# Performance work log

Measured on AMD Instinct MI355X. Metric: run time of the kernel, lower is better.

The kernel has to match this reference:

```python
import jax, jax.numpy as jnp
import numpy as np

B, H, W, C = 4, 256, 256, 128
HEADS, WS, SHIFT = 4, 8, 4
EPS = 1e-5


def _rel_pos_index(ws):
    coords = np.stack(np.meshgrid(np.arange(ws), np.arange(ws), indexing='ij'))
    cf = coords.reshape(2, -1)
    rel = (cf[:, :, None] - cf[:, None, :]).transpose(1, 2, 0)
    rel[:, :, 0] += ws - 1
    rel[:, :, 1] += ws - 1
    rel[:, :, 0] *= 2 * ws - 1
    return rel.sum(-1).reshape(-1)

REL_IDX = jnp.array(_rel_pos_index(WS))


def _shift_mask(h, w, ws, shift):
    img = np.zeros((1, h, w, 1))
    cnt = 0
    sl = (slice(0, -ws), slice(-ws, -shift), slice(-shift, None))
    for hs in sl:
        for wsl in sl:
            img[:, hs, wsl, :] = cnt
            cnt += 1
    m = img.reshape(1, h // ws, ws, w // ws, ws, 1).transpose(0, 1, 3, 2, 4, 5).reshape(-1, ws * ws)
    am = m[:, None, :] - m[:, :, None]
    return jnp.array(np.where(am != 0, -100.0, 0.0).astype(np.float32))

ATTN_MASK = _shift_mask(H, W, WS, SHIFT)  # (nW, ws*ws, ws*ws)


def _ln(x, scale, bias):
    mu = x.mean(-1, keepdims=True)
    var = x.var(-1, keepdims=True)
    return (x - mu) / jnp.sqrt(var + EPS) * scale + bias


def setup_inputs() -> dict:
    key = jax.random.key(0)
    ks = jax.random.split(key, 8)
    s = 0.02
    return dict(
        hidden_states=jax.random.normal(ks[0], (B, H * W, C), jnp.float32),
        ln1_scale=jnp.ones((C,), jnp.float32), ln1_bias=jnp.zeros((C,), jnp.float32),
        q_w=jax.random.normal(ks[1], (C, C), jnp.float32) * s, q_b=jnp.zeros((C,), jnp.float32),
        k_w=jax.random.normal(ks[2], (C, C), jnp.float32) * s, k_b=jnp.zeros((C,), jnp.float32),
        v_w=jax.random.normal(ks[3], (C, C), jnp.float32) * s, v_b=jnp.zeros((C,), jnp.float32),
        proj_w=jax.random.normal(ks[4], (C, C), jnp.float32) * s, proj_b=jnp.zeros((C,), jnp.float32),
        rpb_table=jax.random.normal(ks[5], ((2 * WS - 1) ** 2, HEADS), jnp.float32) * s,
        ln2_scale=jnp.ones((C,), jnp.float32), ln2_bias=jnp.zeros((C,), jnp.float32),
        fc1_w=jax.random.normal(ks[6], (C, 4 * C), jnp.float32) * s, fc1_b=jnp.zeros((4 * C,), jnp.float32),
        fc2_w=jax.random.normal(ks[7], (4 * C, C), jnp.float32) * s, fc2_b=jnp.zeros((C,), jnp.float32),
    )


def reference(hidden_states, ln1_scale, ln1_bias, q_w, q_b, k_w, k_b, v_w, v_b,
              proj_w, proj_b, rpb_table, ln2_scale, ln2_bias, fc1_w, fc1_b, fc2_w, fc2_b):
    hd = C // HEADS
    T = WS * WS
    nW = (H // WS) * (W // WS)
    shortcut = hidden_states
    x = _ln(hidden_states, ln1_scale, ln1_bias).reshape(B, H, W, C)
    # cyclic shift
    x = jnp.roll(x, (-SHIFT, -SHIFT), axis=(1, 2))
    # window partition -> (B*nW, T, C)
    x = x.reshape(B, H // WS, WS, W // WS, WS, C).transpose(0, 1, 3, 2, 4, 5).reshape(-1, T, C)
    q = (x @ q_w + q_b).reshape(-1, T, HEADS, hd) / jnp.sqrt(jnp.float32(hd))
    k = (x @ k_w + k_b).reshape(-1, T, HEADS, hd)
    v = (x @ v_w + v_b).reshape(-1, T, HEADS, hd)
    attn = jnp.einsum('bqhd,bkhd->bhqk', q, k)
    bias = rpb_table[REL_IDX].reshape(T, T, HEADS).transpose(2, 0, 1)  # (h, q, k)
    attn = attn + bias[None]
    # shift mask per window
    attn = attn.reshape(B, nW, HEADS, T, T) + ATTN_MASK[None, :, None]
    attn = jax.nn.softmax(attn.reshape(-1, HEADS, T, T), axis=-1)
    out = jnp.einsum('bhqk,bkhd->bqhd', attn, v).reshape(-1, T, C)
    out = out @ proj_w + proj_b
    # window reverse + un-shift
    out = out.reshape(B, H // WS, W // WS, WS, WS, C).transpose(0, 1, 3, 2, 4, 5).reshape(B, H, W, C)
    out = jnp.roll(out, (SHIFT, SHIFT), axis=(1, 2)).reshape(B, H * W, C)
    x = shortcut + out
    y = _ln(x, ln2_scale, ln2_bias)
    y = jax.nn.gelu(y @ fc1_w + fc1_b, approximate=False) @ fc2_w + fc2_b
    return x + y
```

## Files before the change

kernel.cpp:

```cpp
#include <hip/hip_runtime.h>
#include <hip/hip_bf16.h>
#include <math.h>

#define B_ 4
#define H_ 256
#define W_ 256
#define C_ 128
#define HEADS_ 4
#define HD_ 32
#define WS_ 8
#define SHIFT_ 4
#define T_ 64
#define NW_ 1024
#define M_ (B_*NW_*T_)

typedef float floatx4 __attribute__((ext_vector_type(4)));
typedef short bf16x8 __attribute__((ext_vector_type(8)));
typedef unsigned short ushort8v __attribute__((ext_vector_type(8)));

#define MFMA16(a,b,c) __builtin_amdgcn_mfma_f32_16x16x32_bf16(a,b,c,0,0,0)

__device__ __forceinline__ unsigned short f2b(float f){
    union { float f; unsigned int i; } c; c.f = f;
    unsigned int r = c.i + 0x7FFFu + ((c.i >> 16) & 1u);
    return (unsigned short)(r >> 16);
}
__device__ __forceinline__ int region_id(int x){ return (x < 248) ? 0 : ((x < 252) ? 1 : 2); }

__device__ __forceinline__ bf16x8 ldfrag(const unsigned short* p){
    return *(const bf16x8*)p;
}
__device__ __forceinline__ bf16x8 ldfrag_strided(const unsigned short* p, int stride){
    ushort8v u;
    #pragma unroll
    for (int j = 0; j < 8; j++) u[j] = p[j*stride];
    return __builtin_bit_cast(bf16x8, u);
}
__device__ __forceinline__ floatx4 fzero(){ floatx4 v = {0.f,0.f,0.f,0.f}; return v; }

__device__ __forceinline__ float gelu_fast(float x){
    float z = x * 0.70710678118654752f;
    float az = fabsf(z);
    float t = __builtin_amdgcn_rcpf(fmaf(0.3275911f, az, 1.0f));
    float poly = t*(0.254829592f + t*(-0.284496736f + t*(1.421413741f +
                 t*(-1.453152027f + t*1.061405429f))));
    float e = __expf(-z*z);
    float er = 1.0f - poly*e;
    er = (z < 0.f) ? -er : er;
    return 0.5f * x * (1.0f + er);
}

#define WSO_QT   0
#define WSO_KT   16384
#define WSO_VT   32768
#define WSO_PT   49152
#define WSO_W1T  65536
#define WSO_W2T  131072
#define WSO_BIAS 196608
#define WS_BYTES_NEEDED (196608u*2u + 16384u*4u)

__global__ __launch_bounds__(256) void prep_weights_kernel(
        const float* __restrict__ qw, const float* __restrict__ kw,
        const float* __restrict__ vw, const float* __restrict__ pw,
        const float* __restrict__ fc1, const float* __restrict__ fc2,
        const float* __restrict__ rpb, unsigned short* __restrict__ ws)
{
    int tid = blockIdx.x * 256 + threadIdx.x;
    int nt = gridDim.x * 256;
    for (int i = tid; i < 16384; i += nt) {
        int n = i >> 7, k = i & 127;
        ws[WSO_QT + i] = f2b(qw[k*128 + n]);
        ws[WSO_KT + i] = f2b(kw[k*128 + n]);
        ws[WSO_VT + i] = f2b(vw[k*128 + n]);
        ws[WSO_PT + i] = f2b(pw[k*128 + n]);
    }
    for (int i = tid; i < 65536; i += nt) {
        int n = i >> 7, k = i & 127;
        ws[WSO_W1T + i] = f2b(fc1[(size_t)k*512 + n]);
    }
    for (int i = tid; i < 65536; i += nt) {
        int n = i >> 9, k = i & 511;
        ws[WSO_W2T + i] = f2b(fc2[(size_t)k*128 + n]);
    }
    float* bt = (float*)(ws + WSO_BIAS);
    for (int i = tid; i < 16384; i += nt) {
        int h = i >> 12, q = (i >> 6) & 63, k = i & 63;
        int th = q >> 3, tw = q & 7, jh = k >> 3, jw = k & 7;
        bt[i] = rpb[((th - jh + 7)*15 + (tw - jw + 7))*HEADS_ + h];
    }
}

__device__ __forceinline__ void gemm64x128_g(
        const unsigned short (*Xs)[136], const unsigned short* __restrict__ Wt,
        int wv, int quad, int l15, floatx4 acc[4][2])
{
    #pragma unroll
    for (int c = 0; c < 4; c++) {
        bf16x8 bf0 = ldfrag(Wt + (size_t)(32*wv + l15)*128      + c*32 + quad*8);
        bf16x8 bf1 = ldfrag(Wt + (size_t)(32*wv + 16 + l15)*128 + c*32 + quad*8);
        #pragma unroll
        for (int m = 0; m < 4; m++) {
            bf16x8 af = ldfrag(&Xs[16*m + l15][c*32 + quad*8]);
            acc[m][0] = MFMA16(af, bf0, acc[m][0]);
            acc[m][1] = MFMA16(af, bf1, acc[m][1]);
        }
    }
}

__global__ __launch_bounds__(256, 3) void swin_fused_kernel(
        const float* __restrict__ hidden,
        const float* __restrict__ ln1_s, const float* __restrict__ ln1_b,
        const float* __restrict__ q_b, const float* __restrict__ k_b,
        const float* __restrict__ v_b, const float* __restrict__ p_b,
        const float* __restrict__ ln2_s, const float* __restrict__ ln2_b,
        const float* __restrict__ b1, const float* __restrict__ b2,
        const unsigned short* __restrict__ wsu,
        float* __restrict__ outp)
{
    __shared__ __align__(16) unsigned short SH[2][T_][136];
    __shared__ __align__(16) unsigned short VsT[C_][72];
    unsigned short (*Xs)[136] = SH[0];
    unsigned short (*Ks)[136] = SH[1];

    int tid = threadIdx.x;
    int wv = tid >> 6, lane = tid & 63;
    int quad = lane >> 4, l15 = lane & 15;
    int gw = blockIdx.x;
    int wi = gw & (NW_-1), b = gw >> 10;
    int hb = wi >> 5, wb = wi & 31;

    {
        int rloc = lane >> 2;
        int t = wv*16 + rloc;
        int th = t >> 3, tw = t & 7;
        int h = (hb*8 + th + SHIFT_) & 255;
        int w = (wb*8 + tw + SHIFT_) & 255;
        int c0 = (lane & 3) * 32;
        const float* xp = hidden + ((size_t)((b<<16) + (h<<8) + w)) * C_ + c0;
        float4 xv[8];
        float s = 0.f, ss = 0.f;
        #pragma unroll
        for (int i = 0; i < 8; i++) {
            xv[i] = *((const float4*)xp + i);
            s  += xv[i].x + xv[i].y + xv[i].z + xv[i].w;
            ss += xv[i].x*xv[i].x + xv[i].y*xv[i].y + xv[i].z*xv[i].z + xv[i].w*xv[i].w;
        }
        s  += __shfl_xor(s, 1, 64);  s  += __shfl_xor(s, 2, 64);
        ss += __shfl_xor(ss, 1, 64); ss += __shfl_xor(ss, 2, 64);
        float mean = s * (1.0f/C_);
        float var  = ss * (1.0f/C_) - mean*mean;
        float rstd = __builtin_amdgcn_rsqf(var + 1e-5f);
        #pragma unroll
        for (int i = 0; i < 8; i++) {
            float4 sc = *((const float4*)(ln1_s + c0) + i);
            float4 bi = *((const float4*)(ln1_b + c0) + i);
            ushort4 o;
            o.x = f2b((xv[i].x - mean)*rstd*sc.x + bi.x);
            o.y = f2b((xv[i].y - mean)*rstd*sc.y + bi.y);
            o.z = f2b((xv[i].z - mean)*rstd*sc.z + bi.z);
            o.w = f2b((xv[i].w - mean)*rstd*sc.w + bi.w);
            *(ushort4*)&Xs[t][c0 + 4*i] = o;
        }
    }
    __syncthreads();

    floatx4 qacc[4][2];
    {
        floatx4 kacc[4][2], vacc[4][2];
        #pragma unroll
        for (int m = 0; m < 4; m++) {
            qacc[m][0] = fzero(); qacc[m][1] = fzero();
            kacc[m][0] = fzero(); kacc[m][1] = fzero();
            vacc[m][0] = fzero(); vacc[m][1] = fzero();
        }
        const unsigned short* Qt = wsu + WSO_QT;
        const unsigned short* Kt = wsu + WSO_KT;
        const unsigned short* Vt = wsu + WSO_VT;
        #pragma unroll
        for (int c = 0; c < 4; c++) {
            size_t off0 = (size_t)(32*wv + l15)*128      + c*32 + quad*8;
            size_t off1 = (size_t)(32*wv + 16 + l15)*128 + c*32 + quad*8;
            bf16x8 qf0 = ldfrag(Qt + off0), qf1 = ldfrag(Qt + off1);
            bf16x8 kf0 = ldfrag(Kt + off0), kf1 = ldfrag(Kt + off1);
            bf16x8 vf0 = ldfrag(Vt + off0), vf1 = ldfrag(Vt + off1);
            #pragma unroll
            for (int m = 0; m < 4; m++) {
                bf16x8 af = ldfrag(&Xs[16*m + l15][c*32 + quad*8]);
                qacc[m][0] = MFMA16(af, qf0, qacc[m][0]);
                qacc[m][1] = MFMA16(af, qf1, qacc[m][1]);
                kacc[m][0] = MFMA16(af, kf0, kacc[m][0]);
                kacc[m][1] = MFMA16(af, kf1, kacc[m][1]);
                vacc[m][0] = MFMA16(af, vf0, vacc[m][0]);
                vacc[m][1] = MFMA16(af, vf1, vacc[m][1]);
            }
        }
        float kb0 = k_b[32*wv + l15], kb1 = k_b[32*wv + 16 + l15];
        float vb0 = v_b[32*wv + l15], vb1 = v_b[32*wv + 16 + l15];
        #pragma unroll
        for (int m = 0; m < 4; m++)
            #pragma unroll
            for (int r = 0; r < 4; r++) {
                int q = 16*m + 4*quad + r;
                Ks[q][32*wv + l15]      = f2b(kacc[m][0][r] + kb0);
                Ks[q][32*wv + 16 + l15] = f2b(kacc[m][1][r] + kb1);
                VsT[32*wv + l15][q]      = f2b(vacc[m][0][r] + vb0);
                VsT[32*wv + 16 + l15][q] = f2b(vacc[m][1][r] + vb1);
            }
    }
    __syncthreads();
    {
        const float sc = 0.17677669529663687f;
        float qb0 = q_b[32*wv + l15], qb1 = q_b[32*wv + 16 + l15];
        #pragma unroll
        for (int m = 0; m < 4; m++)
            #pragma unroll
            for (int r = 0; r < 4; r++) {
                int q = 16*m + 4*quad + r;
                Xs[q][32*wv + l15]      = f2b((qacc[m][0][r] + qb0) * sc);
                Xs[q][32*wv + 16 + l15] = f2b((qacc[m][1][r] + qb1) * sc);
            }
    }

    floatx4 sacc[4][4];
    #pragma unroll
    for (int m = 0; m < 4; m++)
        #pragma unroll
        for (int n = 0; n < 4; n++) sacc[m][n] = fzero();
    {
        bf16x8 qf[4], kf[4];
        #pragma unroll
        for (int m = 0; m < 4; m++) qf[m] = ldfrag(&Xs[16*m + l15][32*wv + quad*8]);
        #pragma unroll
        for (int n = 0; n < 4; n++) kf[n] = ldfrag(&Ks[16*n + l15][32*wv + quad*8]);
        #pragma unroll
        for (int m = 0; m < 4; m++)
            #pragma unroll
            for (int n = 0; n < 4; n++) sacc[m][n] = MFMA16(kf[n], qf[m], sacc[m][n]);
    }

    {
        const float* bt = (const float*)(wsu + WSO_BIAS) + (wv << 12);
        int cidk[4][4];
        #pragma unroll
        for (int n = 0; n < 4; n++)
            #pragma unroll
            for (int r = 0; r < 4; r++) {
                int kt = 16*n + 4*quad + r;
                cidk[n][r] = region_id(hb*8 + (kt >> 3))*3 + region_id(wb*8 + (kt & 7));
            }
        #pragma unroll
        for (int m = 0; m < 4; m++) {
            int q = 16*m + l15;
            int cidq = region_id(hb*8 + (q >> 3))*3 + region_id(wb*8 + (q & 7));
            float v[4][4];
            float mx = -3.0e38f;
            #pragma unroll
            for (int n = 0; n < 4; n++) {
                float4 bv = *(const float4*)(bt + q*64 + 16*n + 4*quad);
                #pragma unroll
                for (int r = 0; r < 4; r++) {
                    float d = sacc[m][n][r] + bv[r];
                    if (cidq != cidk[n][r]) d -= 100.f;
                    v[n][r] = d;
                    mx = fmaxf(mx, d);
                }
            }
            mx = fmaxf(mx, __shfl_xor(mx, 16, 64));
            mx = fmaxf(mx, __shfl_xor(mx, 32, 64));
            float sum = 0.f;
            #pragma unroll
            for (int n = 0; n < 4; n++)
                #pragma unroll
                for (int r = 0; r < 4; r++) { v[n][r] = __expf(v[n][r] - mx); sum += v[n][r]; }
            sum += __shfl_xor(sum, 16, 64);
            sum += __shfl_xor(sum, 32, 64);
            float inv = __builtin_amdgcn_rcpf(sum);
            #pragma unroll
            for (int n = 0; n < 4; n++)
                #pragma unroll
                for (int r = 0; r < 4; r++) sacc[m][n][r] = v[n][r] * inv;
        }
    }
    __syncthreads();

    unsigned short* Ph = (wv < 2) ? (&Ks[0][0] + wv*2560) : (&Xs[0][0] + (wv-2)*2560);
    floatx4 oacc[4][2];
    #pragma unroll
    for (int m = 0; m < 4; m++) { oacc[m][0] = fzero(); oacc[m][1] = fzero(); }
    #pragma unroll
    for (int kb = 0; kb < 2; kb++) {
        #pragma unroll
        for (int m = 0; m < 4; m++)
            #pragma unroll
            for (int n2 = 0; n2 < 2; n2++)
                #pragma unroll
                for (int r = 0; r < 4; r++)
                    Ph[(16*m + l15)*40 + n2*16 + 4*quad + r] = f2b(sacc[m][2*kb + n2][r]);
        bf16x8 bf0 = ldfrag(&VsT[32*wv + l15][kb*32 + quad*8]);
        bf16x8 bf1 = ldfrag(&VsT[32*wv + 16 + l15][kb*32 + quad*8]);
        #pragma unroll
        for (int m = 0; m < 4; m++) {
            bf16x8 af = ldfrag(&Ph[(16*m + l15)*40 + quad*8]);
            oacc[m][0] = MFMA16(af, bf0, oacc[m][0]);
            oacc[m][1] = MFMA16(af, bf1, oacc[m][1]);
        }
    }
    __syncthreads();
    #pragma unroll
    for (int m = 0; m < 4; m++)
        #pragma unroll
        for (int r = 0; r < 4; r++) {
            int q = 16*m + 4*quad + r;
            Xs[q][32*wv + l15]      = f2b(oacc[m][0][r]);
            Xs[q][32*wv + 16 + l15] = f2b(oacc[m][1][r]);
        }
    __syncthreads();

    floatx4 pacc[4][2];
    #pragma unroll
    for (int m = 0; m < 4; m++) { pacc[m][0] = fzero(); pacc[m][1] = fzero(); }
    gemm64x128_g(Xs, wsu + WSO_PT, wv, quad, l15, pacc);
    {
        float pb0 = p_b[32*wv + l15], pb1 = p_b[32*wv + 16 + l15];
        #pragma unroll
        for (int m = 0; m < 4; m++)
            #pragma unroll
            for (int r = 0; r < 4; r++) {
                int t = 16*m + 4*quad + r;
                int th = t >> 3, tw = t & 7;
                int h = (hb*8 + th + SHIFT_) & 255;
                int w = (wb*8 + tw + SHIFT_) & 255;
                size_t src = ((size_t)((b<<16) + (h<<8) + w)) * C_;
                pacc[m][0][r] += pb0 + hidden[src + 32*wv + l15];
                pacc[m][1][r] += pb1 + hidden[src + 32*wv + 16 + l15];
            }
    }
    __syncthreads();

    float* Fb = (float*)&SH[0][0][0];
    #pragma unroll
    for (int m = 0; m < 4; m++)
        #pragma unroll
        for (int r = 0; r < 4; r++) {
            int q = 16*m + 4*quad + r;
            Fb[q*132 + 32*wv + l15]      = pacc[m][0][r];
            Fb[q*132 + 32*wv + 16 + l15] = pacc[m][1][r];
        }
    __syncthreads();

    unsigned short (*As)[136] = (unsigned short(*)[136])&VsT[0][0];
    {
        int rloc = lane >> 2;
        int t = wv*16 + rloc;
        int c0 = (lane & 3) * 32;
        const float* xp = Fb + t*132 + c0;
        float4 xv[8];
        float s = 0.f, ss = 0.f;
        #pragma unroll
        for (int i = 0; i < 8; i++) {
            xv[i] = *((const float4*)xp + i);
            s  += xv[i].x + xv[i].y + xv[i].z + xv[i].w;
            ss += xv[i].x*xv[i].x + xv[i].y*xv[i].y + xv[i].z*xv[i].z + xv[i].w*xv[i].w;
        }
        s  += __shfl_xor(s, 1, 64);  s  += __shfl_xor(s, 2, 64);
        ss += __shfl_xor(ss, 1, 64); ss += __shfl_xor(ss, 2, 64);
        float mean = s * (1.0f/C_);
        float var  = ss * (1.0f/C_) - mean*mean;
        float rstd = __builtin_amdgcn_rsqf(var + 1e-5f);
        #pragma unroll
        for (int i = 0; i < 8; i++) {
            float4 sc = *((const float4*)(ln2_s + c0) + i);
            float4 bi = *((const float4*)(ln2_b + c0) + i);
            ushort4 o;
            o.x = f2b((xv[i].x - mean)*rstd*sc.x + bi.x);
            o.y = f2b((xv[i].y - mean)*rstd*sc.y + bi.y);
            o.z = f2b((xv[i].z - mean)*rstd*sc.z + bi.z);
            o.w = f2b((xv[i].w - mean)*rstd*sc.w + bi.w);
            *(ushort4*)&As[t][c0 + 4*i] = o;
        }
    }
    __syncthreads();

    unsigned short (*G)[72] = (unsigned short(*)[72])&SH[0][0][0];
    const unsigned short* W1t = wsu + WSO_W1T;
    const unsigned short* W2t = wsu + WSO_W2T;
    floatx4 acc2[4][2];
    #pragma unroll
    for (int m = 0; m < 4; m++) { acc2[m][0] = fzero(); acc2[m][1] = fzero(); }

    for (int ch = 0; ch < 8; ch++) {
        floatx4 a1[4];
        #pragma unroll
        for (int m = 0; m < 4; m++) a1[m] = fzero();
        #pragma unroll
        for (int kc = 0; kc < 4; kc++) {
            bf16x8 bf = ldfrag(W1t + (size_t)(ch*64 + 16*wv + l15)*128 + kc*32 + quad*8);
            #pragma unroll
            for (int m = 0; m < 4; m++) {
                bf16x8 af = ldfrag(&As[16*m + l15][kc*32 + quad*8]);
                a1[m] = MFMA16(af, bf, a1[m]);
            }
        }
        __syncthreads();
        {
            int c_rel = 16*wv + l15;
            float bb = b1[ch*64 + c_rel];
            #pragma unroll
            for (int m = 0; m < 4; m++)
                #pragma unroll
                for (int r = 0; r < 4; r++) {
                    float hh = a1[m][r] + bb;
                    G[16*m + 4*quad + r][c_rel] = f2b(gelu_fast(hh));
                }
        }
        __syncthreads();
        #pragma unroll
        for (int ki = 0; ki < 2; ki++) {
            bf16x8 bf0 = ldfrag(W2t + (size_t)(32*wv + l15)*512      + ch*64 + ki*32 + quad*8);
            bf16x8 bf1 = ldfrag(W2t + (size_t)(32*wv + 16 + l15)*512 + ch*64 + ki*32 + quad*8);
            #pragma unroll
            for (int m = 0; m < 4; m++) {
                bf16x8 af = ldfrag(&G[16*m + l15][ki*32 + quad*8]);
                acc2[m][0] = MFMA16(af, bf0, acc2[m][0]);
                acc2[m][1] = MFMA16(af, bf1, acc2[m][1]);
            }
        }
    }
    __syncthreads();

    {
        float bb0 = b2[32*wv + l15], bb1 = b2[32*wv + 16 + l15];
        #pragma unroll
        for (int m = 0; m < 4; m++)
            #pragma unroll
            for (int r = 0; r < 4; r++) {
                int q = 16*m + 4*quad + r;
                Fb[q*132 + 32*wv + l15]      = pacc[m][0][r] + acc2[m][0][r] + bb0;
                Fb[q*132 + 32*wv + 16 + l15] = pacc[m][1][r] + acc2[m][1][r] + bb1;
            }
        __syncthreads();
        int t = tid >> 2;
        int cs = (tid & 3) * 32;
        int th = t >> 3, tw = t & 7;
        int h = (hb*8 + th + SHIFT_) & 255;
        int w = (wb*8 + tw + SHIFT_) & 255;
        size_t dst = ((size_t)((b<<16) + (h<<8) + w)) * C_ + cs;
        float4* op = (float4*)(outp + dst);
        const float4* fp = (const float4*)(Fb + t*132 + cs);
        #pragma unroll
        for (int i = 0; i < 8; i++) op[i] = fp[i];
    }
}


__device__ __forceinline__ void gemm64x128(
        const unsigned short (*Xs)[136], unsigned short (*Wc)[132],
        const float* __restrict__ Wg, int tid, int wv, int quad, int l15,
        floatx4 acc[4][2])
{
    for (int c = 0; c < 4; c++) {
        __syncthreads();
        #pragma unroll
        for (int it = 0; it < 4; it++) {
            int idx = tid + it*256;
            int kk = idx >> 5;
            int n4 = (idx & 31) * 4;
            float4 v = *(const float4*)(Wg + (size_t)(c*32 + kk)*C_ + n4);
            ushort4 o; o.x=f2b(v.x); o.y=f2b(v.y); o.z=f2b(v.z); o.w=f2b(v.w);
            *(ushort4*)&Wc[kk][n4] = o;
        }
        __syncthreads();
        bf16x8 bf0 = ldfrag_strided(&Wc[quad*8][32*wv + l15],      132);
        bf16x8 bf1 = ldfrag_strided(&Wc[quad*8][32*wv + 16 + l15], 132);
        #pragma unroll
        for (int m = 0; m < 4; m++) {
            bf16x8 af = ldfrag(&Xs[16*m + l15][c*32 + quad*8]);
            acc[m][0] = MFMA16(af, bf0, acc[m][0]);
            acc[m][1] = MFMA16(af, bf1, acc[m][1]);
        }
    }
}

__global__ __launch_bounds__(256) void swin_attn_kernel(
        const float* __restrict__ hidden,
        const float* __restrict__ ln1_s, const float* __restrict__ ln1_b,
        const float* __restrict__ q_w, const float* __restrict__ q_b,
        const float* __restrict__ k_w, const float* __restrict__ k_b,
        const float* __restrict__ v_w, const float* __restrict__ v_b,
        const float* __restrict__ p_w, const float* __restrict__ p_b,
        const float* __restrict__ rpb,
        float* __restrict__ xres)
{
    __shared__ unsigned short Xs[T_][136];
    __shared__ unsigned short Ks[T_][136];
    __shared__ unsigned short Vs[T_][134];
    __shared__ __align__(16) unsigned char U[10240];

    unsigned short (*Wc)[132] = (unsigned short(*)[132])U;
    float* rpbf = (float*)U;

    int tid = threadIdx.x;
    int wv = tid >> 6, lane = tid & 63;
    int quad = lane >> 4, l15 = lane & 15;
    int gw = blockIdx.x;
    int wi = gw & (NW_-1), b = gw >> 10;
    int hb = wi >> 5, wb = wi & 31;

    for (int it = 0; it < 16; it++) {
        int t = wv*16 + it;
        int th = t >> 3, tw = t & 7;
        int h = (hb*8 + th + SHIFT_) & 255;
        int w = (wb*8 + tw + SHIFT_) & 255;
        size_t src = ((size_t)((b<<16) + (h<<8) + w)) * C_;
        float2 u = *(const float2*)(hidden + src + 2*lane);
        float x0 = u.x, x1 = u.y;
        float s = x0 + x1, ss = x0*x0 + x1*x1;
        #pragma unroll
        for (int m = 32; m > 0; m >>= 1) {
            s  += __shfl_xor(s,  m, 64);
            ss += __shfl_xor(ss, m, 64);
        }
        float mean = s * (1.0f/C_);
        float var  = ss * (1.0f/C_) - mean*mean;
        float rstd = rsqrtf(var + 1e-5f);
        int c0 = 2*lane;
        ushort2 o;
        o.x = f2b((x0 - mean) * rstd * ln1_s[c0]   + ln1_b[c0]);
        o.y = f2b((x1 - mean) * rstd * ln1_s[c0+1] + ln1_b[c0+1]);
        *(ushort2*)&Xs[t][c0] = o;
    }

    {
        floatx4 acc[4][2];
        #pragma unroll
        for (int m = 0; m < 4; m++) { acc[m][0] = fzero(); acc[m][1] = fzero(); }
        gemm64x128(Xs, Wc, k_w, tid, wv, quad, l15, acc);
        float kb0 = k_b[32*wv + l15], kb1 = k_b[32*wv + 16 + l15];
        #pragma unroll
        for (int m = 0; m < 4; m++)
            #pragma unroll
            for (int r = 0; r < 4; r++) {
                int q = 16*m + 4*quad + r;
                Ks[q][32*wv + l15]      = f2b(acc[m][0][r] + kb0);
                Ks[q][32*wv + 16 + l15] = f2b(acc[m][1][r] + kb1);
            }
    }
    {
        floatx4 acc[4][2];
        #pragma unroll
        for (int m = 0; m < 4; m++) { acc[m][0] = fzero(); acc[m][1] = fzero(); }
        gemm64x128(Xs, Wc, v_w, tid, wv, quad, l15, acc);
        float vb0 = v_b[32*wv + l15], vb1 = v_b[32*wv + 16 + l15];
        #pragma unroll
        for (int m = 0; m < 4; m++)
            #pragma unroll
            for (int r = 0; r < 4; r++) {
                int q = 16*m + 4*quad + r;
                Vs[q][32*wv + l15]      = f2b(acc[m][0][r] + vb0);
                Vs[q][32*wv + 16 + l15] = f2b(acc[m][1][r] + vb1);
            }
    }
    floatx4 qacc[4][2];
    #pragma unroll
    for (int m = 0; m < 4; m++) { qacc[m][0] = fzero(); qacc[m][1] = fzero(); }
    gemm64x128(Xs, Wc, q_w, tid, wv, quad, l15, qacc);
    __syncthreads();
    for (int i = tid; i < 225*HEADS_; i += 256) rpbf[i] = rpb[i];
    {
        const float sc = 0.17677669529663687f;
        float qb0 = q_b[32*wv + l15], qb1 = q_b[32*wv + 16 + l15];
        #pragma unroll
        for (int m = 0; m < 4; m++)
            #pragma unroll
            for (int r = 0; r < 4; r++) {
                int q = 16*m + 4*quad + r;
                Xs[q][32*wv + l15]      = f2b((qacc[m][0][r] + qb0) * sc);
                Xs[q][32*wv + 16 + l15] = f2b((qacc[m][1][r] + qb1) * sc);
            }
    }
    __syncthreads();

    floatx4 sacc[4][4];
    #pragma unroll
    for (int m = 0; m < 4; m++)
        #pragma unroll
        for (int n = 0; n < 4; n++) sacc[m][n] = fzero();
    {
        bf16x8 qf[4], kf[4];
        #pragma unroll
        for (int m = 0; m < 4; m++) qf[m] = ldfrag(&Xs[16*m + l15][32*wv + quad*8]);
        #pragma unroll
        for (int n = 0; n < 4; n++) kf[n] = ldfrag(&Ks[16*n + l15][32*wv + quad*8]);
        #pragma unroll
        for (int m = 0; m < 4; m++)
            #pragma unroll
            for (int n = 0; n < 4; n++) sacc[m][n] = MFMA16(qf[m], kf[n], sacc[m][n]);
    }
    {
        int jh_[4], jw_[4], cidj_[4];
        #pragma unroll
        for (int n = 0; n < 4; n++) {
            int kt = 16*n + l15;
            jh_[n] = kt >> 3; jw_[n] = kt & 7;
            cidj_[n] = region_id(hb*8 + jh_[n])*3 + region_id(wb*8 + jw_[n]);
        }
        #pragma unroll
        for (int m = 0; m < 4; m++)
            #pragma unroll
            for (int r = 0; r < 4; r++) {
                int q = 16*m + 4*quad + r;
                int th = q >> 3, twq = q & 7;
                int cidi = region_id(hb*8 + th)*3 + region_id(wb*8 + twq);
                float v[4];
                #pragma unroll
                for (int n = 0; n < 4; n++) {
                    float d = sacc[m][n][r];
                    d += rpbf[((th - jh_[n] + 7)*15 + (twq - jw_[n] + 7))*HEADS_ + wv];
                    if (cidi != cidj_[n]) d -= 100.f;
                    v[n] = d;
                }
                float mx = fmaxf(fmaxf(v[0],v[1]), fmaxf(v[2],v[3]));
                #pragma unroll
                for (int off = 1; off < 16; off <<= 1) mx = fmaxf(mx, __shfl_xor(mx, off, 64));
                float sum = 0.f;
                #pragma unroll
                for (int n = 0; n < 4; n++) { v[n] = __expf(v[n] - mx); sum += v[n]; }
                #pragma unroll
                for (int off = 1; off < 16; off <<= 1) sum += __shfl_xor(sum, off, 64);
                float inv = 1.0f / sum;
                #pragma unroll
                for (int n = 0; n < 4; n++) sacc[m][n][r] = v[n] * inv;
            }
    }
    __syncthreads();

    unsigned short* Ph = (wv < 2) ? (&Ks[0][0] + wv*2560)
                                  : ((unsigned short*)U + (wv-2)*2560);
    floatx4 oacc[4][2];
    #pragma unroll
    for (int m = 0; m < 4; m++) { oacc[m][0] = fzero(); oacc[m][1] = fzero(); }
    for (int kb = 0; kb < 2; kb++) {
        #pragma unroll
        for (int m = 0; m < 4; m++)
            #pragma unroll
            for (int r = 0; r < 4; r++) {
                int q = 16*m + 4*quad + r;
                Ph[q*40 + l15]      = f2b(sacc[m][2*kb+0][r]);
                Ph[q*40 + 16 + l15] = f2b(sacc[m][2*kb+1][r]);
            }
        __syncthreads();
        bf16x8 bf0 = ldfrag_strided(&Vs[kb*32 + quad*8][32*wv + l15],      134);
        bf16x8 bf1 = ldfrag_strided(&Vs[kb*32 + quad*8][32*wv + 16 + l15], 134);
        #pragma unroll
        for (int m = 0; m < 4; m++) {
            bf16x8 af = ldfrag(&Ph[(16*m + l15)*40 + quad*8]);
            oacc[m][0] = MFMA16(af, bf0, oacc[m][0]);
            oacc[m][1] = MFMA16(af, bf1, oacc[m][1]);
        }
        __syncthreads();
    }
    #pragma unroll
    for (int m = 0; m < 4; m++)
        #pragma unroll
        for (int r = 0; r < 4; r++) {
            int q = 16*m + 4*quad + r;
            Xs[q][32*wv + l15]      = f2b(oacc[m][0][r]);
            Xs[q][32*wv + 16 + l15] = f2b(oacc[m][1][r]);
        }
    {
        floatx4 acc[4][2];
        #pragma unroll
        for (int m = 0; m < 4; m++) { acc[m][0] = fzero(); acc[m][1] = fzero(); }
        gemm64x128(Xs, Wc, p_w, tid, wv, quad, l15, acc);
        float pb0 = p_b[32*wv + l15], pb1 = p_b[32*wv + 16 + l15];
        #pragma unroll
        for (int m = 0; m < 4; m++)
            #pragma unroll
            for (int r = 0; r < 4; r++) {
                int t = 16*m + 4*quad + r;
                int th = t >> 3, tw = t & 7;
                int h = (hb*8 + th + SHIFT_) & 255;
                int w = (wb*8 + tw + SHIFT_) & 255;
                size_t dst = ((size_t)((b<<16) + (h<<8) + w)) * C_;
                int c0 = 32*wv + l15;
                xres[dst + c0]      = hidden[dst + c0]      + acc[m][0][r] + pb0;
                xres[dst + c0 + 16] = hidden[dst + c0 + 16] + acc[m][1][r] + pb1;
            }
    }
}

__global__ __launch_bounds__(256) void mlp_ln_kernel(
        float* __restrict__ xio,
        const float* __restrict__ ln2_s, const float* __restrict__ ln2_b,
        const float* __restrict__ W1, const float* __restrict__ b1,
        const float* __restrict__ W2, const float* __restrict__ b2)
{
    __shared__ unsigned short As[T_][136];
    __shared__ unsigned short G[T_][72];
    __shared__ unsigned short W1c[C_][68];
    __shared__ unsigned short W2c[T_][132];
    int tid = threadIdx.x, wv = tid >> 6, lane = tid & 63;
    int quad = lane >> 4, l15 = lane & 15;
    size_t row0 = (size_t)blockIdx.x * 64;

    for (int it = 0; it < 16; it++) {
        int t = wv*16 + it;
        const float* xp = xio + (row0 + t)*C_;
        float2 u = *(const float2*)(xp + 2*lane);
        float x0 = u.x, x1 = u.y;
        float s = x0 + x1, ss = x0*x0 + x1*x1;
        #pragma unroll
        for (int m = 32; m > 0; m >>= 1) {
            s  += __shfl_xor(s,  m, 64);
            ss += __shfl_xor(ss, m, 64);
        }
        float mean = s * (1.0f/C_);
        float var  = ss * (1.0f/C_) - mean*mean;
        float rstd = rsqrtf(var + 1e-5f);
        int c0 = 2*lane;
        ushort2 o;
        o.x = f2b((x0 - mean) * rstd * ln2_s[c0]   + ln2_b[c0]);
        o.y = f2b((x1 - mean) * rstd * ln2_s[c0+1] + ln2_b[c0+1]);
        *(ushort2*)&As[t][c0] = o;
    }

    floatx4 acc2[4][2];
    #pragma unroll
    for (int m = 0; m < 4; m++) { acc2[m][0] = fzero(); acc2[m][1] = fzero(); }

    for (int ch = 0; ch < 8; ch++) {
        __syncthreads();
        #pragma unroll
        for (int it = 0; it < 8; it++) {
            int idx = tid + it*256;
            int k = idx >> 4, n4 = (idx & 15) * 4;
            float4 v = *(const float4*)(W1 + (size_t)k*512 + ch*64 + n4);
            ushort4 o; o.x=f2b(v.x); o.y=f2b(v.y); o.z=f2b(v.z); o.w=f2b(v.w);
            *(ushort4*)&W1c[k][n4] = o;
        }
        #pragma unroll
        for (int it = 0; it < 8; it++) {
            int idx = tid + it*256;
            int k = idx >> 5, n4 = (idx & 31) * 4;
            float4 v = *(const float4*)(W2 + (size_t)(ch*64 + k)*C_ + n4);
            ushort4 o; o.x=f2b(v.x); o.y=f2b(v.y); o.z=f2b(v.z); o.w=f2b(v.w);
            *(ushort4*)&W2c[k][n4] = o;
        }
        __syncthreads();
        floatx4 a1[4];
        #pragma unroll
        for (int m = 0; m < 4; m++) a1[m] = fzero();
        #pragma unroll
        for (int kc = 0; kc < 4; kc++) {
            bf16x8 bfrag = ldfrag_strided(&W1c[kc*32 + quad*8][16*wv + l15], 68);
            #pragma unroll
            for (int m = 0; m < 4; m++) {
                bf16x8 af = ldfrag(&As[16*m + l15][kc*32 + quad*8]);
                a1[m] = MFMA16(af, bfrag, a1[m]);
            }
        }
        {
            int c_rel = 16*wv + l15;
            float bb = b1[ch*64 + c_rel];
            #pragma unroll
            for (int m = 0; m < 4; m++)
                #pragma unroll
                for (int r = 0; r < 4; r++) {
                    int q = 16*m + 4*quad + r;
                    float hh = a1[m][r] + bb;
                    float g = 0.5f * hh * (1.0f + erff(hh * 0.70710678118654752f));
                    G[q][c_rel] = f2b(g);
                }
        }
        __syncthreads();
        #pragma unroll
        for (int ki = 0; ki < 2; ki++) {
            bf16x8 bf0 = ldfrag_strided(&W2c[ki*32 + quad*8][32*wv + l15],      132);
            bf16x8 bf1 = ldfrag_strided(&W2c[ki*32 + quad*8][32*wv + 16 + l15], 132);
            #pragma unroll
            for (int m = 0; m < 4; m++) {
                bf16x8 af = ldfrag(&G[16*m + l15][ki*32 + quad*8]);
                acc2[m][0] = MFMA16(af, bf0, acc2[m][0]);
                acc2[m][1] = MFMA16(af, bf1, acc2[m][1]);
            }
        }
    }
    {
        float bb0 = b2[32*wv + l15], bb1 = b2[32*wv + 16 + l15];
        #pragma unroll
        for (int m = 0; m < 4; m++)
            #pragma unroll
            for (int r = 0; r < 4; r++) {
                size_t rr = row0 + 16*m + 4*quad + r;
                int c0 = 32*wv + l15;
                xio[rr*C_ + c0]      += acc2[m][0][r] + bb0;
                xio[rr*C_ + c0 + 16] += acc2[m][1][r] + bb1;
            }
    }
}

extern "C" void kernel_launch(void* const* d_in, const int* in_sizes, int n_in,
                              void* d_out, int out_size, void* d_ws, size_t ws_size,
                              hipStream_t stream) {
    (void)in_sizes; (void)n_in; (void)out_size;
    const float* hidden = (const float*)d_in[0];
    const float* ln1_s  = (const float*)d_in[1];
    const float* ln1_b  = (const float*)d_in[2];
    const float* q_w    = (const float*)d_in[3];
    const float* q_b    = (const float*)d_in[4];
    const float* k_w    = (const float*)d_in[5];
    const float* k_b    = (const float*)d_in[6];
    const float* v_w    = (const float*)d_in[7];
    const float* v_b    = (const float*)d_in[8];
    const float* p_w    = (const float*)d_in[9];
    const float* p_b    = (const float*)d_in[10];
    const float* rpb    = (const float*)d_in[11];
    const float* ln2_s  = (const float*)d_in[12];
    const float* ln2_b  = (const float*)d_in[13];
    const float* fc1_w  = (const float*)d_in[14];
    const float* fc1_b  = (const float*)d_in[15];
    const float* fc2_w  = (const float*)d_in[16];
    const float* fc2_b  = (const float*)d_in[17];
    float* outp = (float*)d_out;

    if (d_ws != nullptr && ws_size >= (size_t)WS_BYTES_NEEDED) {
        unsigned short* wsu = (unsigned short*)d_ws;
        prep_weights_kernel<<<64, 256, 0, stream>>>(q_w, k_w, v_w, p_w,
                fc1_w, fc2_w, rpb, wsu);
        swin_fused_kernel<<<B_*NW_, 256, 0, stream>>>(hidden, ln1_s, ln1_b,
                q_b, k_b, v_b, p_b, ln2_s, ln2_b, fc1_b, fc2_b, wsu, outp);
    } else {
        swin_attn_kernel<<<B_*NW_, 256, 0, stream>>>(hidden, ln1_s, ln1_b,
                q_w, q_b, k_w, k_b, v_w, v_b, p_w, p_b, rpb, outp);
        mlp_ln_kernel<<<M_/64, 256, 0, stream>>>(outp, ln2_s, ln2_b,
                fc1_w, fc1_b, fc2_w, fc2_b);
    }
}
```

Before: 568.2 us.

## Shrink fused Swin kernel LDS footprint to raise occupancy to four blocks

Replaces the separate shared arrays with one 40 KB byte buffer that aliases K, V-transpose, P, LN2 input and the final staging tile, and raises the launch bound from 3 to 4 blocks per CU. V is kept packed in registers and written to LDS only after the score MFMAs, using vectorised uint2 stores. LN2 now computes mean and rstd from a padded float tile and normalises directly from the accumulator registers. The weight-prep kernel switches to coalesced reads and a larger grid. The trade-off is more register pressure under the tighter launch bound, plus an extra barrier, with a risk of spills.

```diff
diff --git a/kernel.cpp b/kernel.cpp
--- a/kernel.cpp
+++ b/kernel.cpp
@@ -68,19 +68,20 @@
     int tid = blockIdx.x * 256 + threadIdx.x;
     int nt = gridDim.x * 256;
     for (int i = tid; i < 16384; i += nt) {
-        int n = i >> 7, k = i & 127;
-        ws[WSO_QT + i] = f2b(qw[k*128 + n]);
-        ws[WSO_KT + i] = f2b(kw[k*128 + n]);
-        ws[WSO_VT + i] = f2b(vw[k*128 + n]);
-        ws[WSO_PT + i] = f2b(pw[k*128 + n]);
+        int k = i >> 7, n = i & 127;
+        int o = n*128 + k;
+        ws[WSO_QT + o] = f2b(qw[i]);
+        ws[WSO_KT + o] = f2b(kw[i]);
+        ws[WSO_VT + o] = f2b(vw[i]);
+        ws[WSO_PT + o] = f2b(pw[i]);
     }
     for (int i = tid; i < 65536; i += nt) {
-        int n = i >> 7, k = i & 127;
-        ws[WSO_W1T + i] = f2b(fc1[(size_t)k*512 + n]);
+        int k = i >> 9, n = i & 511;
+        ws[WSO_W1T + n*128 + k] = f2b(fc1[i]);
     }
     for (int i = tid; i < 65536; i += nt) {
-        int n = i >> 9, k = i & 511;
-        ws[WSO_W2T + i] = f2b(fc2[(size_t)k*128 + n]);
+        int k = i >> 7, n = i & 127;
+        ws[WSO_W2T + n*512 + k] = f2b(fc2[i]);
     }
     float* bt = (float*)(ws + WSO_BIAS);
     for (int i = tid; i < 16384; i += nt) {
@@ -107,7 +108,7 @@
     }
 }
 
-__global__ __launch_bounds__(256, 3) void swin_fused_kernel(
+__global__ __launch_bounds__(256, 4) void swin_fused_kernel(
         const float* __restrict__ hidden,
         const float* __restrict__ ln1_s, const float* __restrict__ ln1_b,
         const float* __restrict__ q_b, const float* __restrict__ k_b,
@@ -117,10 +118,10 @@
         const unsigned short* __restrict__ wsu,
         float* __restrict__ outp)
 {
-    __shared__ __align__(16) unsigned short SH[2][T_][136];
-    __shared__ __align__(16) unsigned short VsT[C_][72];
-    unsigned short (*Xs)[136] = SH[0];
-    unsigned short (*Ks)[136] = SH[1];
+    __shared__ __align__(16) unsigned char LDS[40960];
+    unsigned short (*Xs)[136] = (unsigned short(*)[136])LDS;
+    unsigned short (*Ks)[136] = (unsigned short(*)[136])(LDS + 17408);
+    unsigned short (*VsT)[72] = (unsigned short(*)[72])(LDS + 17408);
 
     int tid = threadIdx.x;
     int wv = tid >> 6, lane = tid & 63;
@@ -165,6 +166,7 @@
     __syncthreads();
 
     floatx4 qacc[4][2];
+    unsigned int vpk[4][2][2];
     {
         floatx4 kacc[4][2], vacc[4][2];
         #pragma unroll
@@ -197,15 +199,22 @@
         float kb0 = k_b[32*wv + l15], kb1 = k_b[32*wv + 16 + l15];
         float vb0 = v_b[32*wv + l15], vb1 = v_b[32*wv + 16 + l15];
         #pragma unroll
-        for (int m = 0; m < 4; m++)
+        for (int m = 0; m < 4; m++) {
             #pragma unroll
             for (int r = 0; r < 4; r++) {
                 int q = 16*m + 4*quad + r;
                 Ks[q][32*wv + l15]      = f2b(kacc[m][0][r] + kb0);
                 Ks[q][32*wv + 16 + l15] = f2b(kacc[m][1][r] + kb1);
-                VsT[32*wv + l15][q]      = f2b(vacc[m][0][r] + vb0);
-                VsT[32*wv + 16 + l15][q] = f2b(vacc[m][1][r] + vb1);
-            }
+            }
+            vpk[m][0][0] = (unsigned int)f2b(vacc[m][0][0] + vb0)
+                         | ((unsigned int)f2b(vacc[m][0][1] + vb0) << 16);
+            vpk[m][0][1] = (unsigned int)f2b(vacc[m][0][2] + vb0)
+                         | ((unsigned int)f2b(vacc[m][0][3] + vb0) << 16);
+            vpk[m][1][0] = (unsigned int)f2b(vacc[m][1][0] + vb1)
+                         | ((unsigned int)f2b(vacc[m][1][1] + vb1) << 16);
+            vpk[m][1][1] = (unsigned int)f2b(vacc[m][1][2] + vb1)
+                         | ((unsigned int)f2b(vacc[m][1][3] + vb1) << 16);
+        }
     }
     __syncthreads();
     {
@@ -237,6 +246,15 @@
             #pragma unroll
             for (int n = 0; n < 4; n++) sacc[m][n] = MFMA16(kf[n], qf[m], sacc[m][n]);
     }
+    __syncthreads();
+
+    #pragma unroll
+    for (int m = 0; m < 4; m++)
+        #pragma unroll
+        for (int u = 0; u < 2; u++) {
+            uint2 p; p.x = vpk[m][u][0]; p.y = vpk[m][u][1];
+            *(uint2*)&VsT[32*wv + 16*u + l15][16*m + 4*quad] = p;
+        }
 
     {
         const float* bt = (const float*)(wsu + WSO_BIAS) + (wv << 12);
@@ -281,9 +299,8 @@
                 for (int r = 0; r < 4; r++) sacc[m][n][r] = v[n][r] * inv;
         }
     }
-    __syncthreads();
-
-    unsigned short* Ph = (wv < 2) ? (&Ks[0][0] + wv*2560) : (&Xs[0][0] + (wv-2)*2560);
+
+    unsigned short* Ph = (unsigned short*)(LDS + (wv < 3 ? wv*5120 : 35840));
     floatx4 oacc[4][2];
     #pragma unroll
     for (int m = 0; m < 4; m++) { oacc[m][0] = fzero(); oacc[m][1] = fzero(); }
@@ -337,51 +354,55 @@
     }
     __syncthreads();
 
-    float* Fb = (float*)&SH[0][0][0];
+    float* Fb = (float*)LDS;
     #pragma unroll
     for (int m = 0; m < 4; m++)
         #pragma unroll
         for (int r = 0; r < 4; r++) {
             int q = 16*m + 4*quad + r;
-            Fb[q*132 + 32*wv + l15]      = pacc[m][0][r];
-            Fb[q*132 + 32*wv + 16 + l15] = pacc[m][1][r];
-        }
-    __syncthreads();
-
-    unsigned short (*As)[136] = (unsigned short(*)[136])&VsT[0][0];
-    {
-        int rloc = lane >> 2;
+            Fb[q*140 + wv*36 + l15]      = pacc[m][0][r];
+            Fb[q*140 + wv*36 + 16 + l15] = pacc[m][1][r];
+        }
+    __syncthreads();
+
+    float* RB = (float*)(LDS + 35840);
+    {
+        int rloc = lane >> 2, seg = lane & 3;
         int t = wv*16 + rloc;
-        int c0 = (lane & 3) * 32;
-        const float* xp = Fb + t*132 + c0;
-        float4 xv[8];
+        const float4* fp = (const float4*)(Fb + t*140 + seg*36);
         float s = 0.f, ss = 0.f;
         #pragma unroll
         for (int i = 0; i < 8; i++) {
-            xv[i] = *((const float4*)xp + i);
-            s  += xv[i].x + xv[i].y + xv[i].z + xv[i].w;
-            ss += xv[i].x*xv[i].x + xv[i].y*xv[i].y + xv[i].z*xv[i].z + xv[i].w*xv[i].w;
+            float4 v = fp[i];
+            s  += v.x + v.y + v.z + v.w;
+            ss += v.x*v.x + v.y*v.y + v.z*v.z + v.w*v.w;
         }
         s  += __shfl_xor(s, 1, 64);  s  += __shfl_xor(s, 2, 64);
         ss += __shfl_xor(ss, 1, 64); ss += __shfl_xor(ss, 2, 64);
         float mean = s * (1.0f/C_);
         float var  = ss * (1.0f/C_) - mean*mean;
         float rstd = __builtin_amdgcn_rsqf(var + 1e-5f);
-        #pragma unroll
-        for (int i = 0; i < 8; i++) {
-            float4 sc = *((const float4*)(ln2_s + c0) + i);
-            float4 bi = *((const float4*)(ln2_b + c0) + i);
-            ushort4 o;
-            o.x = f2b((xv[i].x - mean)*rstd*sc.x + bi.x);
-            o.y = f2b((xv[i].y - mean)*rstd*sc.y + bi.y);
-            o.z = f2b((xv[i].z - mean)*rstd*sc.z + bi.z);
-            o.w = f2b((xv[i].w - mean)*rstd*sc.w + bi.w);
-            *(ushort4*)&As[t][c0 + 4*i] = o;
-        }
-    }
-    __syncthreads();
-
-    unsigned short (*G)[72] = (unsigned short(*)[72])&SH[0][0][0];
+        if (seg == 0) { float2 mr; mr.x = mean; mr.y = rstd; *(float2*)&RB[2*t] = mr; }
+    }
+    __syncthreads();
+
+    unsigned short (*As)[136] = Ks;
+    {
+        float s0 = ln2_s[32*wv + l15],      s1 = ln2_s[32*wv + 16 + l15];
+        float e0 = ln2_b[32*wv + l15],      e1 = ln2_b[32*wv + 16 + l15];
+        #pragma unroll
+        for (int m = 0; m < 4; m++)
+            #pragma unroll
+            for (int r = 0; r < 4; r++) {
+                int q = 16*m + 4*quad + r;
+                float2 mr = *(const float2*)&RB[2*q];
+                As[q][32*wv + l15]      = f2b((pacc[m][0][r] - mr.x)*mr.y*s0 + e0);
+                As[q][32*wv + 16 + l15] = f2b((pacc[m][1][r] - mr.x)*mr.y*s1 + e1);
+            }
+    }
+    __syncthreads();
+
+    unsigned short (*G)[72] = (unsigned short(*)[72])LDS;
     const unsigned short* W1t = wsu + WSO_W1T;
     const unsigned short* W2t = wsu + WSO_W2T;
     floatx4 acc2[4][2];
@@ -435,18 +456,18 @@
             #pragma unroll
             for (int r = 0; r < 4; r++) {
                 int q = 16*m + 4*quad + r;
-                Fb[q*132 + 32*wv + l15]      = pacc[m][0][r] + acc2[m][0][r] + bb0;
-                Fb[q*132 + 32*wv + 16 + l15] = pacc[m][1][r] + acc2[m][1][r] + bb1;
+                Fb[q*140 + wv*36 + l15]      = pacc[m][0][r] + acc2[m][0][r] + bb0;
+                Fb[q*140 + wv*36 + 16 + l15] = pacc[m][1][r] + acc2[m][1][r] + bb1;
             }
         __syncthreads();
         int t = tid >> 2;
-        int cs = (tid & 3) * 32;
+        int seg = tid & 3;
         int th = t >> 3, tw = t & 7;
         int h = (hb*8 + th + SHIFT_) & 255;
         int w = (wb*8 + tw + SHIFT_) & 255;
-        size_t dst = ((size_t)((b<<16) + (h<<8) + w)) * C_ + cs;
+        size_t dst = ((size_t)((b<<16) + (h<<8) + w)) * C_ + seg*32;
         float4* op = (float4*)(outp + dst);
-        const float4* fp = (const float4*)(Fb + t*132 + cs);
+        const float4* fp = (const float4*)(Fb + t*140 + seg*36);
         #pragma unroll
         for (int i = 0; i < 8; i++) op[i] = fp[i];
     }
@@ -825,7 +846,7 @@
 
     if (d_ws != nullptr && ws_size >= (size_t)WS_BYTES_NEEDED) {
         unsigned short* wsu = (unsigned short*)d_ws;
-        prep_weights_kernel<<<64, 256, 0, stream>>>(q_w, k_w, v_w, p_w,
+        prep_weights_kernel<<<256, 256, 0, stream>>>(q_w, k_w, v_w, p_w,
                 fc1_w, fc2_w, rpb, wsu);
         swin_fused_kernel<<<B_*NW_, 256, 0, stream>>>(hidden, ln1_s, ln1_b,
                 q_b, k_b, v_b, p_b, ln2_s, ln2_b, fc1_b, fc2_b, wsu, outp);
```

New measurement: 598.4 us. 5.3% more time.
